# Optimization experiments

Measured on AMD Instinct MI355X. Metric: run time of the kernel, lower is better.

The kernel has to match this reference:

```python
import jax, jax.numpy as jnp
import numpy as np

NS_STEPS = 10
NS_A, NS_B, NS_C = 3.4445, -4.7750, 2.0315  # standard quintic Newton-Schulz coefficients
EPS = 1e-7

def orthogonalize(w):
    """Newton-Schulz iteration producing a (near-)orthogonal matrix from w."""
    din, dout = w.shape
    transpose = din > dout  # iterate on the wide orientation so X @ X.T is small
    x = w.T if transpose else w
    x = x / (jnp.linalg.norm(x) + EPS)  # spectral norm <= frobenius norm -> contraction

    def body(x, _):
        a = x @ x.T                      # (m, m) Gram matrix
        bmat = NS_B * a + NS_C * (a @ a)
        x = NS_A * x + bmat @ x
        return x, None

    x, _ = jax.lax.scan(body, x, None, length=NS_STEPS)
    return x.T if transpose else x


def setup_inputs() -> dict:
    key = jax.random.key(0)
    k1, k2, k3 = jax.random.split(key, 3)
    B, DIN, DOUT = 16384, 2048, 2048
    x = jax.random.normal(k1, (B, DIN), dtype=jnp.float32)
    w = jax.random.normal(k2, (DIN, DOUT), dtype=jnp.float32)
    b = jax.random.normal(k3, (DOUT,), dtype=jnp.float32) * 0.02
    return {"x": x, "w": w, "b": b}


def reference(x, w, b):
    w_orth = orthogonalize(w)
    return x @ w_orth + b
```

## Files before the change

kernel.cpp:

```cpp
#include <hip/hip_runtime.h>
#include <stdint.h>

typedef unsigned short u16;
typedef _Float16 half_t;
typedef __attribute__((ext_vector_type(4))) float f32x4;
typedef __attribute__((ext_vector_type(8))) _Float16 f16x8;

#define NS_A 3.4445f
#define NS_B -4.7750f
#define NS_C 2.0315f

#define SX      64.0f
#define INV_SX  (1.0f / 64.0f)
#define INV_SA  (1.0f / 4096.0f)

typedef const __attribute__((address_space(1))) void* as1_cvp;
typedef __attribute__((address_space(3))) void* as3_vp;
#define GLOAD_LDS16(gp, lp) \
    __builtin_amdgcn_global_load_lds((as1_cvp)(const void*)(gp), (as3_vp)(void*)(lp), 16, 0, 0)

#define BK 64

template <int MODE, bool SWZ, int BMt, int BNt>
__global__ __launch_bounds__(256, 3) void gemm_nt(
    const half_t* __restrict__ A, const half_t* __restrict__ B,
    const half_t* __restrict__ aux, const float* __restrict__ bias,
    void* __restrict__ outp, half_t* __restrict__ outpT,
    int M, int N, int K)
{
    constexpr int M_REP = BMt / 32;
    constexpr int N_REP = BNt / 32;

    __shared__ half_t As[2][BMt * BK];
    __shared__ half_t Bs[2][BNt * BK];
    const int tid  = threadIdx.x;
    const int wave = tid >> 6;
    const int lane = tid & 63;

    int bid = blockIdx.x;
    if (SWZ) {
        const int cpx = gridDim.x >> 3;
        bid = (bid & 7) * cpx + (bid >> 3);
    }
    const int nbx  = N / BNt;
    const int brow = (bid / nbx) * BMt;
    const int bcol = (bid % nbx) * BNt;
    const int wr = wave >> 1, wc = wave & 1;

    f32x4 acc[M_REP][N_REP] = {};

    const int r0  = tid >> 3;
    const int c8s = (((tid & 7) ^ ((tid >> 3) & 7))) * 8;

    const half_t* gA = A + (size_t)(brow + r0) * K + c8s;
    const half_t* gB = B + (size_t)(bcol + r0) * K + c8s;

    auto stage = [&](int buf, int kt) {
#pragma unroll
        for (int j = 0; j < BMt / 32; ++j)
            GLOAD_LDS16(gA + (size_t)(j * 32) * K + kt, &As[buf][(size_t)(j * 256 + wave * 64) * 8]);
#pragma unroll
        for (int j = 0; j < BNt / 32; ++j)
            GLOAD_LDS16(gB + (size_t)(j * 32) * K + kt, &Bs[buf][(size_t)(j * 256 + wave * 64) * 8]);
    };

    stage(0, 0);
    __syncthreads();

    const int nsteps = K / BK;
    for (int s = 0; s < nsteps; ++s) {
        const int cur = s & 1;
        if (s + 1 < nsteps) stage(cur ^ 1, (s + 1) * BK);

        f16x8 af[M_REP][2], bfr[N_REP][2];
#pragma unroll
        for (int m = 0; m < M_REP; ++m) {
            const int row = wr * (BMt / 2) + m * 16 + (lane & 15);
#pragma unroll
            for (int kk = 0; kk < 2; ++kk) {
                const int cc = (kk * 4 + (lane >> 4)) ^ (row & 7);
                af[m][kk] = *(const f16x8*)&As[cur][row * BK + cc * 8];
            }
        }
#pragma unroll
        for (int n = 0; n < N_REP; ++n) {
            const int row = wc * (BNt / 2) + n * 16 + (lane & 15);
#pragma unroll
            for (int kk = 0; kk < 2; ++kk) {
                const int cc = (kk * 4 + (lane >> 4)) ^ (row & 7);
                bfr[n][kk] = *(const f16x8*)&Bs[cur][row * BK + cc * 8];
            }
        }
#pragma unroll
        for (int kk = 0; kk < 2; ++kk)
#pragma unroll
            for (int m = 0; m < M_REP; ++m)
#pragma unroll
                for (int n = 0; n < N_REP; ++n)
                    acc[m][n] = __builtin_amdgcn_mfma_f32_16x16x32_f16(af[m][kk], bfr[n][kk], acc[m][n], 0, 0, 0);

        __syncthreads();
    }

#pragma unroll
    for (int m = 0; m < M_REP; ++m) {
#pragma unroll
        for (int n = 0; n < N_REP; ++n) {
            const int row0 = brow + wr * (BMt / 2) + m * 16 + (lane >> 4) * 4;
            const int col  = bcol + wc * (BNt / 2) + n * 16 + (lane & 15);
#pragma unroll
            for (int r = 0; r < 4; ++r) {
                const size_t idx = (size_t)(row0 + r) * N + col;
                const float v = acc[m][n][r];
                if (MODE == 0) {
                    ((half_t*)outp)[idx] = (half_t)v;
                } else if (MODE == 1) {
                    ((half_t*)outp)[idx] = (half_t)(NS_B * (float)aux[idx] + NS_C * v * INV_SA);
                } else if (MODE == 2) {
                    const half_t o = (half_t)(NS_A * (float)aux[idx] + v * INV_SA);
                    ((half_t*)outp)[idx] = o;
                    if (outpT) outpT[(size_t)col * M + row0 + r] = o;
                } else {
                    ((float*)outp)[idx] = v * INV_SX + bias[col];
                }
            }
        }
    }
}

__global__ __launch_bounds__(256) void k_sumsq(const float* __restrict__ w,
                                               float* __restrict__ part, int n) {
    __shared__ float s[256];
    const int per  = n / 1024;
    const int base = blockIdx.x * per;
    float acc = 0.f;
    for (int i = threadIdx.x; i < per; i += 256) {
        float v = w[base + i];
        acc += v * v;
    }
    s[threadIdx.x] = acc;
    __syncthreads();
    for (int k = 128; k > 0; k >>= 1) {
        if (threadIdx.x < k) s[threadIdx.x] += s[threadIdx.x + k];
        __syncthreads();
    }
    if (threadIdx.x == 0) part[blockIdx.x] = s[0];
}

__global__ __launch_bounds__(256) void k_scalefin(const float* __restrict__ part,
                                                  float* __restrict__ scale) {
    __shared__ float s[256];
    float acc = 0.f;
    for (int i = threadIdx.x; i < 1024; i += 256) acc += part[i];
    s[threadIdx.x] = acc;
    __syncthreads();
    for (int k = 128; k > 0; k >>= 1) {
        if (threadIdx.x < k) s[threadIdx.x] += s[threadIdx.x + k];
        __syncthreads();
    }
    if (threadIdx.x == 0) scale[0] = SX / (sqrtf(s[0]) + 1e-7f);
}

__global__ __launch_bounds__(256) void k_scale_f16(const float* __restrict__ w,
                                                   const float* __restrict__ scale,
                                                   half_t* __restrict__ o, int n) {
    const int i = (blockIdx.x * 256 + threadIdx.x) * 4;
    if (i < n) {
        const float sc = scale[0];
        float4 v = *(const float4*)(w + i);
        o[i + 0] = (half_t)(v.x * sc);
        o[i + 1] = (half_t)(v.y * sc);
        o[i + 2] = (half_t)(v.z * sc);
        o[i + 3] = (half_t)(v.w * sc);
    }
}

__global__ __launch_bounds__(256) void k_cast_f16(const float* __restrict__ w,
                                                  half_t* __restrict__ o, int n) {
    const int i = (blockIdx.x * 256 + threadIdx.x) * 4;
    if (i < n) {
        float4 v = *(const float4*)(w + i);
        o[i + 0] = (half_t)v.x;
        o[i + 1] = (half_t)v.y;
        o[i + 2] = (half_t)v.z;
        o[i + 3] = (half_t)v.w;
    }
}

__global__ __launch_bounds__(256) void k_transpose(const u16* __restrict__ in,
                                                   u16* __restrict__ out, int n) {
    __shared__ u16 tile[64][65];
    const int bx = blockIdx.x * 64, by = blockIdx.y * 64;
    const int tx = threadIdx.x & 63, ty = threadIdx.x >> 6;
    for (int i = ty; i < 64; i += 4) tile[i][tx] = in[(size_t)(by + i) * n + bx + tx];
    __syncthreads();
    for (int i = ty; i < 64; i += 4) out[(size_t)(bx + i) * n + by + tx] = tile[tx][i];
}

extern "C" void kernel_launch(void* const* d_in, const int* in_sizes, int n_in,
                              void* d_out, int out_size, void* d_ws, size_t ws_size,
                              hipStream_t stream) {
    const float* x = (const float*)d_in[0];
    const float* w = (const float*)d_in[1];
    const float* b = (const float*)d_in[2];
    float* out = (float*)d_out;

    const int D  = 2048;
    const int Bm = in_sizes[0] / D;
    const int WN = D * D;
    const int XN = Bm * D;

    const size_t matB = (size_t)WN * 2;
    const bool pingpong = ws_size >= 8192 + 6 * matB + (size_t)XN * 2;

    char* ws = (char*)d_ws;
    float* part  = (float*)ws;
    float* scale = part + 1024;
    half_t* xb0  = (half_t*)(ws + 8192);
    half_t* xb1  = xb0 + WN;
    half_t* xbTa = xb1 + WN;
    half_t* xbTb = pingpong ? (xbTa + WN) : xbTa;
    half_t* amat = xbTb + WN;
    half_t* bmat = amat + WN;
    half_t* xinb = bmat + WN;

    k_sumsq<<<1024, 256, 0, stream>>>(w, part, WN);
    k_scalefin<<<1, 256, 0, stream>>>(part, scale);
    k_scale_f16<<<WN / 4 / 256, 256, 0, stream>>>(w, scale, xb0, WN);

    k_cast_f16<<<XN / 4 / 256, 256, 0, stream>>>(x, xinb, XN);

    const dim3 tgrid(D / 64, D / 64);
    k_transpose<<<tgrid, 256, 0, stream>>>((const u16*)xb0, (u16*)xbTa, D);

    const int ns_grid = (D / 64) * (D / 128);

    half_t* cur = xb0;
    half_t* nxt = xb1;
    half_t* Tr  = xbTa;
    half_t* Tw  = xbTb;
    for (int it = 0; it < 10; ++it) {
        gemm_nt<0, true, 64, 128><<<ns_grid, 256, 0, stream>>>(cur, cur, nullptr, nullptr, amat, nullptr, D, D, D);
        gemm_nt<1, true, 64, 128><<<ns_grid, 256, 0, stream>>>(amat, amat, amat, nullptr, bmat, nullptr, D, D, D);
        if (pingpong) {
            gemm_nt<2, true, 64, 128><<<ns_grid, 256, 0, stream>>>(bmat, Tr, cur, nullptr, nxt, Tw, D, D, D);
            half_t* tt = Tr; Tr = Tw; Tw = tt;
        } else {
            gemm_nt<2, true, 64, 128><<<ns_grid, 256, 0, stream>>>(bmat, Tr, cur, nullptr, nxt, nullptr, D, D, D);
            k_transpose<<<tgrid, 256, 0, stream>>>((const u16*)nxt, (u16*)Tr, D);
        }
        half_t* t = cur; cur = nxt; nxt = t;
    }

    const int fin_grid = (Bm / 128) * (D / 128);
    gemm_nt<3, true, 128, 128><<<fin_grid, 256, 0, stream>>>(xinb, Tr, nullptr, b, out, nullptr, Bm, D, D);
}
```

Baseline: 1.124 ms.

## Exploit symmetry of Gram matrices in Newton-Schulz with upper-triangular GEMM kernel

Adds a symmetric NT GEMM kernel that computes only upper-triangular 64x64 tiles of X·Xᵀ and A·A and mirrors each result into the lower triangle. The two symmetric products in every Newton-Schulz iteration launch this kernel over D/64·(D/64+1)/2 blocks, roughly halving their MMA work. The kernel uses 64x64 tiles instead of 64x128, so per-block reuse drops. The mirrored write of the lower triangle is strided and uncoalesced, and a sqrt-based mapping from block index to triangle tile is added.

```diff
diff --git a/kernel.cpp b/kernel.cpp
--- a/kernel.cpp
+++ b/kernel.cpp
@@ -112,17 +112,114 @@
             for (int r = 0; r < 4; ++r) {
                 const size_t idx = (size_t)(row0 + r) * N + col;
                 const float v = acc[m][n][r];
-                if (MODE == 0) {
-                    ((half_t*)outp)[idx] = (half_t)v;
-                } else if (MODE == 1) {
-                    ((half_t*)outp)[idx] = (half_t)(NS_B * (float)aux[idx] + NS_C * v * INV_SA);
-                } else if (MODE == 2) {
+                if (MODE == 2) {
                     const half_t o = (half_t)(NS_A * (float)aux[idx] + v * INV_SA);
                     ((half_t*)outp)[idx] = o;
                     if (outpT) outpT[(size_t)col * M + row0 + r] = o;
                 } else {
                     ((float*)outp)[idx] = v * INV_SX + bias[col];
                 }
+            }
+        }
+    }
+}
+
+template <int MODE>
+__global__ __launch_bounds__(256, 3) void gemm_nt_sym(
+    const half_t* __restrict__ A, const half_t* __restrict__ aux,
+    half_t* __restrict__ outp, int N, int K)
+{
+    __shared__ half_t As[2][64 * BK];
+    __shared__ half_t Bs[2][64 * BK];
+    const int tid  = threadIdx.x;
+    const int wave = tid >> 6;
+    const int lane = tid & 63;
+
+    int bid = blockIdx.x;
+    {
+        const int cpx = gridDim.x >> 3;
+        bid = (bid & 7) * cpx + (bid >> 3);
+    }
+    int bi = (int)(32.5f - sqrtf(32.5f * 32.5f - 2.0f * (float)bid));
+    bi = bi < 0 ? 0 : (bi > 31 ? 31 : bi);
+    while (bi < 31 && (32 * (bi + 1) - ((bi + 1) * bi) / 2) <= bid) ++bi;
+    while (bi > 0 && (32 * bi - (bi * (bi - 1)) / 2) > bid) --bi;
+    const int bj = bi + (bid - (32 * bi - (bi * (bi - 1)) / 2));
+
+    const int brow = bi * 64;
+    const int bcol = bj * 64;
+    const int wr = wave >> 1, wc = wave & 1;
+
+    f32x4 acc[2][2] = {};
+
+    const int r0  = tid >> 3;
+    const int c8s = (((tid & 7) ^ ((tid >> 3) & 7))) * 8;
+
+    const half_t* gA = A + (size_t)(brow + r0) * K + c8s;
+    const half_t* gB = A + (size_t)(bcol + r0) * K + c8s;
+
+    auto stage = [&](int buf, int kt) {
+#pragma unroll
+        for (int j = 0; j < 2; ++j) {
+            GLOAD_LDS16(gA + (size_t)(j * 32) * K + kt, &As[buf][(size_t)(j * 256 + wave * 64) * 8]);
+            GLOAD_LDS16(gB + (size_t)(j * 32) * K + kt, &Bs[buf][(size_t)(j * 256 + wave * 64) * 8]);
+        }
+    };
+
+    stage(0, 0);
+    __syncthreads();
+
+    const int nsteps = K / BK;
+    for (int s = 0; s < nsteps; ++s) {
+        const int cur = s & 1;
+        if (s + 1 < nsteps) stage(cur ^ 1, (s + 1) * BK);
+
+        f16x8 af[2][2], bfr[2][2];
+#pragma unroll
+        for (int m = 0; m < 2; ++m) {
+            const int row = wr * 32 + m * 16 + (lane & 15);
+#pragma unroll
+            for (int kk = 0; kk < 2; ++kk) {
+                const int cc = (kk * 4 + (lane >> 4)) ^ (row & 7);
+                af[m][kk] = *(const f16x8*)&As[cur][row * BK + cc * 8];
+            }
+        }
+#pragma unroll
+        for (int n = 0; n < 2; ++n) {
+            const int row = wc * 32 + n * 16 + (lane & 15);
+#pragma unroll
+            for (int kk = 0; kk < 2; ++kk) {
+                const int cc = (kk * 4 + (lane >> 4)) ^ (row & 7);
+                bfr[n][kk] = *(const f16x8*)&Bs[cur][row * BK + cc * 8];
+            }
+        }
+#pragma unroll
+        for (int kk = 0; kk < 2; ++kk)
+#pragma unroll
+            for (int m = 0; m < 2; ++m)
+#pragma unroll
+                for (int n = 0; n < 2; ++n)
+                    acc[m][n] = __builtin_amdgcn_mfma_f32_16x16x32_f16(af[m][kk], bfr[n][kk], acc[m][n], 0, 0, 0);
+
+        __syncthreads();
+    }
+
+#pragma unroll
+    for (int m = 0; m < 2; ++m) {
+#pragma unroll
+        for (int n = 0; n < 2; ++n) {
+            const int row0 = brow + wr * 32 + m * 16 + (lane >> 4) * 4;
+            const int col  = bcol + wc * 32 + n * 16 + (lane & 15);
+#pragma unroll
+            for (int r = 0; r < 4; ++r) {
+                const int row = row0 + r;
+                const size_t idx = (size_t)row * N + col;
+                const float v = acc[m][n][r];
+                half_t o;
+                if (MODE == 0) o = (half_t)v;
+                else           o = (half_t)(NS_B * (float)aux[idx] + NS_C * v * INV_SA);
+                if (row <= col) outp[idx] = o;
+                if (row < col)  outp[(size_t)col * N + row] = o;
             }
         }
     }
@@ -233,15 +330,16 @@
     const dim3 tgrid(D / 64, D / 64);
     k_transpose<<<tgrid, 256, 0, stream>>>((const u16*)xb0, (u16*)xbTa, D);
 
-    const int ns_grid = (D / 64) * (D / 128);
+    const int ns_grid  = (D / 64) * (D / 128);
+    const int sym_grid = (D / 64) * (D / 64 + 1) / 2;
 
     half_t* cur = xb0;
     half_t* nxt = xb1;
     half_t* Tr  = xbTa;
     half_t* Tw  = xbTb;
     for (int it = 0; it < 10; ++it) {
-        gemm_nt<0, true, 64, 128><<<ns_grid, 256, 0, stream>>>(cur, cur, nullptr, nullptr, amat, nullptr, D, D, D);
-        gemm_nt<1, true, 64, 128><<<ns_grid, 256, 0, stream>>>(amat, amat, amat, nullptr, bmat, nullptr, D, D, D);
+        gemm_nt_sym<0><<<sym_grid, 256, 0, stream>>>(cur, nullptr, amat, D, D);
+        gemm_nt_sym<1><<<sym_grid, 256, 0, stream>>>(amat, amat, bmat, D, D);
         if (pingpong) {
             gemm_nt<2, true, 64, 128><<<ns_grid, 256, 0, stream>>>(bmat, Tr, cur, nullptr, nxt, Tw, D, D, D);
             half_t* tt = Tr; Tr = Tw; Tw = tt;
```

Result: no change. 1.132 ms (+0.8%).

## Add dedicated 256x256-tile 4-stage pipelined GEMM for final projection

Applied to the files above, without the earlier changes.

Swaps the final x @ W_orth + b GEMM from the generic 128x128, 256-thread kernel to a new 512-thread kernel with 256x256 block tiles. The new kernel uses a 4-slot LDS ring fed by direct global-to-LDS loads, with explicit vmcnt waits, and an XCD-aware block remap. The aim is more data reuse per tile and better overlap of loads with MFMA in the dominant GEMM. In exchange it uses more LDS and registers, so occupancy is lower. The K-loop is hardcoded to steps of 32 and assumes K/32 minus 4 divides by 4, and it has no LDS swizzle, so bank conflicts are possible.

```diff
diff --git a/kernel.cpp b/kernel.cpp
--- a/kernel.cpp
+++ b/kernel.cpp
@@ -128,6 +128,95 @@
     }
 }
 
+__global__ __launch_bounds__(512, 2) void gemm_fin(
+    const half_t* __restrict__ A, const half_t* __restrict__ B,
+    const float* __restrict__ bias, float* __restrict__ out,
+    int M, int N, int K)
+{
+    __shared__ half_t As[4][256 * 32];
+    __shared__ half_t Bs[4][256 * 32];
+    const int tid  = threadIdx.x;
+    const int wid  = tid >> 6;
+    const int lane = tid & 63;
+    const int wm = wid >> 2;
+    const int wn = wid & 3;
+
+    int bid = blockIdx.x;
+    const int cpx = gridDim.x >> 3;
+    bid = (bid & 7) * cpx + (bid >> 3);
+    const int nbx  = N >> 8;
+    const int brow = (bid / nbx) << 8;
+    const int bcol = (bid % nbx) << 8;
+
+    f32x4 acc[8][4] = {};
+
+    const half_t* gA = A + (size_t)(brow + (tid >> 2)) * K + (tid & 3) * 8;
+    const half_t* gB = B + (size_t)(bcol + (tid >> 2)) * K + (tid & 3) * 8;
+
+    int kt_next = 96;
+    auto stage = [&](int slot, int kt) {
+#pragma unroll
+        for (int j = 0; j < 2; ++j)
+            GLOAD_LDS16(gA + (size_t)(j * 128) * K + kt, &As[slot][(j * 512 + wid * 64) * 8]);
+#pragma unroll
+        for (int j = 0; j < 2; ++j)
+            GLOAD_LDS16(gB + (size_t)(j * 128) * K + kt, &Bs[slot][(j * 512 + wid * 64) * 8]);
+    };
+    auto compute = [&](int slot) {
+        f16x8 af[8], bf[4];
+#pragma unroll
+        for (int fr = 0; fr < 8; ++fr)
+            af[fr] = *(const f16x8*)&As[slot][(wm * 128 + fr * 16 + (lane & 15)) * 32 + (lane >> 4) * 8];
+#pragma unroll
+        for (int fc = 0; fc < 4; ++fc)
+            bf[fc] = *(const f16x8*)&Bs[slot][(wn * 64 + fc * 16 + (lane & 15)) * 32 + (lane >> 4) * 8];
+#pragma unroll
+        for (int fr = 0; fr < 8; ++fr)
+#pragma unroll
+            for (int fc = 0; fc < 4; ++fc)
+                acc[fr][fc] = __builtin_amdgcn_mfma_f32_16x16x32_f16(af[fr], bf[fc], acc[fr][fc], 0, 0, 0);
+    };
+
+    stage(0, 0);
+    stage(1, 32);
+    stage(2, 64);
+
+#define FIN_STEP(SLOT, DOSTAGE, VMN) \
+    do { \
+        if (DOSTAGE) { stage((SLOT + 3) & 3, kt_next); kt_next += 32; } \
+        asm volatile("s_waitcnt vmcnt(" #VMN ")" ::: "memory"); \
+        __builtin_amdgcn_s_barrier(); \
+        compute(SLOT); \
+        __builtin_amdgcn_s_barrier(); \
+    } while (0)
+
+    const int nouter = ((K >> 5) - 4) >> 2;
+    for (int tt = 0; tt < nouter; ++tt) {
+        FIN_STEP(0, true, 12);
+        FIN_STEP(1, true, 12);
+        FIN_STEP(2, true, 12);
+        FIN_STEP(3, true, 12);
+    }
+    FIN_STEP(0, true, 12);
+    FIN_STEP(1, false, 8);
+    FIN_STEP(2, false, 4);
+    FIN_STEP(3, false, 0);
+#undef FIN_STEP
+
+#pragma unroll
+    for (int fr = 0; fr < 8; ++fr) {
+#pragma unroll
+        for (int fc = 0; fc < 4; ++fc) {
+            const int row0 = brow + wm * 128 + fr * 16 + (lane >> 4) * 4;
+            const int col  = bcol + wn * 64 + fc * 16 + (lane & 15);
+            const float bv = bias[col];
+#pragma unroll
+            for (int r = 0; r < 4; ++r)
+                out[(size_t)(row0 + r) * N + col] = acc[fr][fc][r] * INV_SX + bv;
+        }
+    }
+}
+
 __global__ __launch_bounds__(256) void k_sumsq(const float* __restrict__ w,
                                                float* __restrict__ part, int n) {
     __shared__ float s[256];
@@ -252,6 +341,6 @@
         half_t* t = cur; cur = nxt; nxt = t;
     }
 
-    const int fin_grid = (Bm / 128) * (D / 128);
-    gemm_nt<3, true, 128, 128><<<fin_grid, 256, 0, stream>>>(xinb, Tr, nullptr, b, out, nullptr, Bm, D, D);
-}
+    const int fin_grid = (Bm / 256) * (D / 256);
+    gemm_fin<<<fin_grid, 512, 0, stream>>>(xinb, Tr, b, out, Bm, D, D);
+}
```

Result: no change. 1.117 ms (-0.6%).

## Replace double-buffered GEMM with 4-slot ring pipeline and larger final tile

Applied to the files above, without the earlier changes.

The double-buffered BK=64 GEMM is replaced by a 4-slot ring of BK=32 stages. Three stages are kept in flight, using explicit vmcnt waits and raw barriers instead of __syncthreads, and MFMA issue priority is raised with setprio. The final x@W GEMM moves to 256x256 tiles with 8 waves to improve data reuse. The goal is to hide global-load latency better and to cut the final GEMM's memory traffic. In exchange, LDS use and register pressure go up, and the larger tile shrinks the final grid.

```diff
diff --git a/kernel.cpp b/kernel.cpp
--- a/kernel.cpp
+++ b/kernel.cpp
@@ -19,99 +19,124 @@
 #define GLOAD_LDS16(gp, lp) \
     __builtin_amdgcn_global_load_lds((as1_cvp)(const void*)(gp), (as3_vp)(void*)(lp), 16, 0, 0)
 
-#define BK 64
-
-template <int MODE, bool SWZ, int BMt, int BNt>
-__global__ __launch_bounds__(256, 3) void gemm_nt(
+template <int N> __device__ __forceinline__ void vmwait() {
+    if constexpr (N == 0)       asm volatile("s_waitcnt vmcnt(0)" ::: "memory");
+    else if constexpr (N == 3)  asm volatile("s_waitcnt vmcnt(3)" ::: "memory");
+    else if constexpr (N == 4)  asm volatile("s_waitcnt vmcnt(4)" ::: "memory");
+    else if constexpr (N == 6)  asm volatile("s_waitcnt vmcnt(6)" ::: "memory");
+    else if constexpr (N == 8)  asm volatile("s_waitcnt vmcnt(8)" ::: "memory");
+    else if constexpr (N == 9)  asm volatile("s_waitcnt vmcnt(9)" ::: "memory");
+    else if constexpr (N == 12) asm volatile("s_waitcnt vmcnt(12)" ::: "memory");
+    else static_assert(N == 0, "unsupported vmcnt");
+}
+
+template <int MODE, int BMt, int BNt, int WAVES_M, int WAVES_N>
+__global__ __launch_bounds__(WAVES_M * WAVES_N * 64, (WAVES_M * WAVES_N == 4) ? 3 : 2)
+void gemm_ring(
     const half_t* __restrict__ A, const half_t* __restrict__ B,
     const half_t* __restrict__ aux, const float* __restrict__ bias,
     void* __restrict__ outp, half_t* __restrict__ outpT,
     int M, int N, int K)
 {
-    constexpr int M_REP = BMt / 32;
-    constexpr int N_REP = BNt / 32;
-
-    __shared__ half_t As[2][BMt * BK];
-    __shared__ half_t Bs[2][BNt * BK];
+    constexpr int THREADS = WAVES_M * WAVES_N * 64;
+    constexpr int M_REP = BMt / WAVES_M / 16;
+    constexpr int N_REP = BNt / WAVES_N / 16;
+    constexpr int LA = (BMt * 4) / THREADS;
+    constexpr int LB = (BNt * 4) / THREADS;
+    constexpr int L  = LA + LB;
+
+    __shared__ half_t As[4][BMt * 32];
+    __shared__ half_t Bs[4][BNt * 32];
     const int tid  = threadIdx.x;
-    const int wave = tid >> 6;
+    const int wid  = tid >> 6;
     const int lane = tid & 63;
+    const int wm = wid / WAVES_N;
+    const int wn = wid % WAVES_N;
 
     int bid = blockIdx.x;
-    if (SWZ) {
-        const int cpx = gridDim.x >> 3;
-        bid = (bid & 7) * cpx + (bid >> 3);
-    }
+    const int cpx = gridDim.x >> 3;
+    bid = (bid & 7) * cpx + (bid >> 3);
     const int nbx  = N / BNt;
     const int brow = (bid / nbx) * BMt;
     const int bcol = (bid % nbx) * BNt;
-    const int wr = wave >> 1, wc = wave & 1;
 
     f32x4 acc[M_REP][N_REP] = {};
 
-    const int r0  = tid >> 3;
-    const int c8s = (((tid & 7) ^ ((tid >> 3) & 7))) * 8;
-
-    const half_t* gA = A + (size_t)(brow + r0) * K + c8s;
-    const half_t* gB = B + (size_t)(bcol + r0) * K + c8s;
-
-    auto stage = [&](int buf, int kt) {
-#pragma unroll
-        for (int j = 0; j < BMt / 32; ++j)
-            GLOAD_LDS16(gA + (size_t)(j * 32) * K + kt, &As[buf][(size_t)(j * 256 + wave * 64) * 8]);
-#pragma unroll
-        for (int j = 0; j < BNt / 32; ++j)
-            GLOAD_LDS16(gB + (size_t)(j * 32) * K + kt, &Bs[buf][(size_t)(j * 256 + wave * 64) * 8]);
+    const int r0   = tid >> 2;
+    const int csrc = ((tid & 3) ^ ((tid >> 3) & 3)) * 8;
+
+    const half_t* gA = A + (size_t)(brow + r0) * K + csrc;
+    const half_t* gB = B + (size_t)(bcol + r0) * K + csrc;
+
+    auto stage = [&](int slot, int kt) {
+#pragma unroll
+        for (int j = 0; j < LA; ++j)
+            GLOAD_LDS16(gA + (size_t)(j * (THREADS / 4)) * K + kt,
+                        &As[slot][(j * THREADS + wid * 64) * 8]);
+#pragma unroll
+        for (int j = 0; j < LB; ++j)
+            GLOAD_LDS16(gB + (size_t)(j * (THREADS / 4)) * K + kt,
+                        &Bs[slot][(j * THREADS + wid * 64) * 8]);
     };
 
+    auto compute = [&](int slot) {
+        f16x8 af[M_REP], bf[N_REP];
+#pragma unroll
+        for (int fr = 0; fr < M_REP; ++fr) {
+            const int row = wm * (BMt / WAVES_M) + fr * 16 + (lane & 15);
+            af[fr] = *(const f16x8*)&As[slot][row * 32 + (((lane >> 4) ^ ((row >> 1) & 3)) * 8)];
+        }
+#pragma unroll
+        for (int fc = 0; fc < N_REP; ++fc) {
+            const int row = wn * (BNt / WAVES_N) + fc * 16 + (lane & 15);
+            bf[fc] = *(const f16x8*)&Bs[slot][row * 32 + (((lane >> 4) ^ ((row >> 1) & 3)) * 8)];
+        }
+        __builtin_amdgcn_s_setprio(1);
+#pragma unroll
+        for (int fr = 0; fr < M_REP; ++fr)
+#pragma unroll
+            for (int fc = 0; fc < N_REP; ++fc)
+                acc[fr][fc] = __builtin_amdgcn_mfma_f32_16x16x32_f16(af[fr], bf[fc], acc[fr][fc], 0, 0, 0);
+        __builtin_amdgcn_s_setprio(0);
+    };
+
     stage(0, 0);
-    __syncthreads();
-
-    const int nsteps = K / BK;
-    for (int s = 0; s < nsteps; ++s) {
-        const int cur = s & 1;
-        if (s + 1 < nsteps) stage(cur ^ 1, (s + 1) * BK);
-
-        f16x8 af[M_REP][2], bfr[N_REP][2];
-#pragma unroll
-        for (int m = 0; m < M_REP; ++m) {
-            const int row = wr * (BMt / 2) + m * 16 + (lane & 15);
-#pragma unroll
-            for (int kk = 0; kk < 2; ++kk) {
-                const int cc = (kk * 4 + (lane >> 4)) ^ (row & 7);
-                af[m][kk] = *(const f16x8*)&As[cur][row * BK + cc * 8];
-            }
-        }
-#pragma unroll
-        for (int n = 0; n < N_REP; ++n) {
-            const int row = wc * (BNt / 2) + n * 16 + (lane & 15);
-#pragma unroll
-            for (int kk = 0; kk < 2; ++kk) {
-                const int cc = (kk * 4 + (lane >> 4)) ^ (row & 7);
-                bfr[n][kk] = *(const f16x8*)&Bs[cur][row * BK + cc * 8];
-            }
-        }
-#pragma unroll
-        for (int kk = 0; kk < 2; ++kk)
-#pragma unroll
-            for (int m = 0; m < M_REP; ++m)
-#pragma unroll
-                for (int n = 0; n < N_REP; ++n)
-                    acc[m][n] = __builtin_amdgcn_mfma_f32_16x16x32_f16(af[m][kk], bfr[n][kk], acc[m][n], 0, 0, 0);
-
-        __syncthreads();
-    }
-
-#pragma unroll
-    for (int m = 0; m < M_REP; ++m) {
-#pragma unroll
-        for (int n = 0; n < N_REP; ++n) {
-            const int row0 = brow + wr * (BMt / 2) + m * 16 + (lane >> 4) * 4;
-            const int col  = bcol + wc * (BNt / 2) + n * 16 + (lane & 15);
+    stage(1, 32);
+    stage(2, 64);
+    int kt_next = 96;
+
+#define RSTEP(SLOT, DOSTAGE, VMN) \
+    do { \
+        if (DOSTAGE) { stage((SLOT + 3) & 3, kt_next); kt_next += 32; } \
+        vmwait<VMN>(); \
+        __builtin_amdgcn_s_barrier(); \
+        compute(SLOT); \
+        __builtin_amdgcn_s_barrier(); \
+    } while (0)
+
+    const int nouter = ((K >> 5) - 4) >> 2;
+    for (int tt = 0; tt < nouter; ++tt) {
+        RSTEP(0, true, 3 * L);
+        RSTEP(1, true, 3 * L);
+        RSTEP(2, true, 3 * L);
+        RSTEP(3, true, 3 * L);
+    }
+    RSTEP(0, true, 3 * L);
+    RSTEP(1, false, 2 * L);
+    RSTEP(2, false, L);
+    RSTEP(3, false, 0);
+#undef RSTEP
+
+#pragma unroll
+    for (int fr = 0; fr < M_REP; ++fr) {
+#pragma unroll
+        for (int fc = 0; fc < N_REP; ++fc) {
+            const int row0 = brow + wm * (BMt / WAVES_M) + fr * 16 + (lane >> 4) * 4;
+            const int col  = bcol + wn * (BNt / WAVES_N) + fc * 16 + (lane & 15);
 #pragma unroll
             for (int r = 0; r < 4; ++r) {
                 const size_t idx = (size_t)(row0 + r) * N + col;
-                const float v = acc[m][n][r];
+                const float v = acc[fr][fc][r];
                 if (MODE == 0) {
                     ((half_t*)outp)[idx] = (half_t)v;
                 } else if (MODE == 1) {
@@ -240,18 +265,18 @@
     half_t* Tr  = xbTa;
     half_t* Tw  = xbTb;
     for (int it = 0; it < 10; ++it) {
-        gemm_nt<0, true, 64, 128><<<ns_grid, 256, 0, stream>>>(cur, cur, nullptr, nullptr, amat, nullptr, D, D, D);
-        gemm_nt<1, true, 64, 128><<<ns_grid, 256, 0, stream>>>(amat, amat, amat, nullptr, bmat, nullptr, D, D, D);
+        gemm_ring<0, 64, 128, 2, 2><<<ns_grid, 256, 0, stream>>>(cur, cur, nullptr, nullptr, amat, nullptr, D, D, D);
+        gemm_ring<1, 64, 128, 2, 2><<<ns_grid, 256, 0, stream>>>(amat, amat, amat, nullptr, bmat, nullptr, D, D, D);
         if (pingpong) {
-            gemm_nt<2, true, 64, 128><<<ns_grid, 256, 0, stream>>>(bmat, Tr, cur, nullptr, nxt, Tw, D, D, D);
+            gemm_ring<2, 64, 128, 2, 2><<<ns_grid, 256, 0, stream>>>(bmat, Tr, cur, nullptr, nxt, Tw, D, D, D);
             half_t* tt = Tr; Tr = Tw; Tw = tt;
         } else {
-            gemm_nt<2, true, 64, 128><<<ns_grid, 256, 0, stream>>>(bmat, Tr, cur, nullptr, nxt, nullptr, D, D, D);
+            gemm_ring<2, 64, 128, 2, 2><<<ns_grid, 256, 0, stream>>>(bmat, Tr, cur, nullptr, nxt, nullptr, D, D, D);
             k_transpose<<<tgrid, 256, 0, stream>>>((const u16*)nxt, (u16*)Tr, D);
         }
         half_t* t = cur; cur = nxt; nxt = t;
     }
 
-    const int fin_grid = (Bm / 128) * (D / 128);
-    gemm_nt<3, true, 128, 128><<<fin_grid, 256, 0, stream>>>(xinb, Tr, nullptr, b, out, nullptr, Bm, D, D);
-}
+    const int fin_grid = (Bm / 256) * (D / 256);
+    gemm_ring<3, 256, 256, 2, 4><<<fin_grid, 512, 0, stream>>>(xinb, Tr, nullptr, b, out, nullptr, Bm, D, D);
+}
```

Measured after the change: 1.314 ms. 16.9% more time.
